# Kernel tuning notes

Hardware: AMD Instinct MI355X
Metric: run time of the kernel (lower is better)

Reference implementation:

```python
import jax, jax.numpy as jnp
import numpy as np

NUM_CODES = 128
CODE_DIM = 64
B, D, T = 64, 64, 8192


def setup_inputs() -> dict:
    key = jax.random.key(0)
    k1, k2 = jax.random.split(key)
    z_e = jax.random.normal(k1, (B, D, T), dtype=jnp.float32)
    centroids = jax.random.normal(k2, (NUM_CODES, CODE_DIM), dtype=jnp.float32)
    return {"z_e": z_e, "centroids": centroids}


def reference(z_e, centroids):
    b, d, t = z_e.shape
    K = centroids.shape[0]
    # [B, D, T] -> [B*T, D]
    z = jnp.transpose(z_e, (0, 2, 1)).reshape(b * t, d)
    # squared euclidean distances: ||z||^2 - 2 z C^T + ||C||^2  -> [N, K]
    dists = (
        jnp.sum(z * z, axis=1, keepdims=True)
        - 2.0 * (z @ centroids.T)
        + jnp.sum(centroids * centroids, axis=1)[None, :]
    )
    idx = jnp.argmin(dists, axis=1)  # [N]
    idx_bt = idx.reshape(b, t)[:, None, :]  # [B, 1, T]
    counts = jnp.bincount(idx, length=K).astype(jnp.float32)  # [K]
    p = jnp.maximum(counts / float(idx.size), 1e-12)
    H = -jnp.sum(p * jnp.log(p))
    perp = jnp.exp(H)
    usage = jnp.mean((counts > 0).astype(jnp.float32))
    return idx_bt, perp, usage
```

## Files before the change

### kernel.cpp

```cpp
#include <hip/hip_runtime.h>
#include <math.h>

#define NUM_CODES 128
#define CODE_DIM  64
#define B_ 64
#define D_ 64
#define T_ 8192
#define N_TOK (B_ * T_)

__global__ __launch_bounds__(128) void kmeans_prep(
    const float* __restrict__ centroids, float* __restrict__ c2h,
    unsigned int* __restrict__ counts)
{
    int k = threadIdx.x;
    if (k < NUM_CODES) {
        const float* cp = centroids + k * CODE_DIM;
        float s0 = 0.f, s1 = 0.f, s2 = 0.f, s3 = 0.f;
        #pragma unroll
        for (int d = 0; d < CODE_DIM; d += 4) {
            s0 = fmaf(cp[d + 0], cp[d + 0], s0);
            s1 = fmaf(cp[d + 1], cp[d + 1], s1);
            s2 = fmaf(cp[d + 2], cp[d + 2], s2);
            s3 = fmaf(cp[d + 3], cp[d + 3], s3);
        }
        c2h[k] = 0.5f * ((s0 + s1) + (s2 + s3));
        counts[k] = 0u;
    }
}

__global__ __launch_bounds__(256) void kmeans_assign(
    const float* __restrict__ z_e, const float* __restrict__ centroids,
    const float* __restrict__ c2h, unsigned int* __restrict__ counts,
    float* __restrict__ out_idx)
{
    const int n = blockIdx.x * 256 + threadIdx.x;
    const int b = n >> 13;
    const int t = n & (T_ - 1);

    const float* zp = z_e + (size_t)b * (size_t)(D_ * T_) + t;
    float z[64];
    #pragma unroll
    for (int d = 0; d < 64; ++d) z[d] = zp[(size_t)d * T_];

    float best = -3.4e38f;
    int   bi   = 0;

    for (int k = 0; k < NUM_CODES; ++k) {
        const float* cp = centroids + k * CODE_DIM;
        float a0 = -c2h[k], a1 = 0.f, a2 = 0.f, a3 = 0.f;
        #pragma unroll
        for (int d = 0; d < 64; d += 4) {
            a0 = fmaf(cp[d + 0], z[d + 0], a0);
            a1 = fmaf(cp[d + 1], z[d + 1], a1);
            a2 = fmaf(cp[d + 2], z[d + 2], a2);
            a3 = fmaf(cp[d + 3], z[d + 3], a3);
        }
        float m = (a0 + a1) + (a2 + a3);
        if (m > best) { best = m; bi = k; }
    }

    out_idx[n] = (float)bi;

    __shared__ unsigned int hist[NUM_CODES];
    if (threadIdx.x < NUM_CODES) hist[threadIdx.x] = 0u;
    __syncthreads();
    atomicAdd(&hist[bi], 1u);
    __syncthreads();
    if (threadIdx.x < NUM_CODES) {
        unsigned int h = hist[threadIdx.x];
        if (h) atomicAdd(&counts[threadIdx.x], h);
    }
}

__global__ __launch_bounds__(128) void kmeans_finalize(
    const unsigned int* __restrict__ counts, float* __restrict__ out)
{
    const int k = threadIdx.x;
    unsigned int c = counts[k];
    float p = fmaxf((float)c * (1.0f / (float)N_TOK), 1e-12f);
    float h = -p * logf(p);
    float u = (c > 0u) ? 1.0f : 0.0f;

    __shared__ float sh[NUM_CODES];
    __shared__ float su[NUM_CODES];
    sh[k] = h; su[k] = u;
    __syncthreads();
    for (int s = 64; s > 0; s >>= 1) {
        if (k < s) { sh[k] += sh[k + s]; su[k] += su[k + s]; }
        __syncthreads();
    }
    if (k == 0) {
        out[N_TOK + 0] = expf(sh[0]);
        out[N_TOK + 1] = su[0] * (1.0f / 128.f);
    }
}

extern "C" void kernel_launch(void* const* d_in, const int* in_sizes, int n_in,
                              void* d_out, int out_size, void* d_ws, size_t ws_size,
                              hipStream_t stream)
{
    const float* z_e       = (const float*)d_in[0];
    const float* centroids = (const float*)d_in[1];
    float* out = (float*)d_out;

    float*        c2h    = (float*)d_ws;
    unsigned int* counts = (unsigned int*)d_ws + NUM_CODES;

    kmeans_prep<<<1, 128, 0, stream>>>(centroids, c2h, counts);
    kmeans_assign<<<N_TOK / 256, 256, 0, stream>>>(z_e, centroids, c2h, counts, out);
    kmeans_finalize<<<1, 128, 0, stream>>>(counts, out);
}
```

Measured before the change: 310.7 us.

## Stage transposed centroids in LDS and split codes across waves per token

The prep kernel now also writes a transposed [D][K] copy of the centroids to the workspace. Each assign block loads that copy into shared memory, and each of its four waves handles 32 codes for the same 64 tokens, keeping per-code accumulators in registers. Partial argmins are then merged through shared memory. This replaces scalar centroid loads from global memory with vectorized LDS reads and removes the 64-float z register array, at the cost of four times as many blocks, a per-block 32KB LDS fill, and each z element being reloaded by all four waves.

```diff
diff --git a/kernel.cpp b/kernel.cpp
--- a/kernel.cpp
+++ b/kernel.cpp
@@ -10,65 +10,102 @@
 
 __global__ __launch_bounds__(128) void kmeans_prep(
     const float* __restrict__ centroids, float* __restrict__ c2h,
-    unsigned int* __restrict__ counts)
+    unsigned int* __restrict__ counts, float* __restrict__ ct)
 {
     int k = threadIdx.x;
-    if (k < NUM_CODES) {
-        const float* cp = centroids + k * CODE_DIM;
-        float s0 = 0.f, s1 = 0.f, s2 = 0.f, s3 = 0.f;
-        #pragma unroll
-        for (int d = 0; d < CODE_DIM; d += 4) {
-            s0 = fmaf(cp[d + 0], cp[d + 0], s0);
-            s1 = fmaf(cp[d + 1], cp[d + 1], s1);
-            s2 = fmaf(cp[d + 2], cp[d + 2], s2);
-            s3 = fmaf(cp[d + 3], cp[d + 3], s3);
-        }
-        c2h[k] = 0.5f * ((s0 + s1) + (s2 + s3));
-        counts[k] = 0u;
+    const float* cp = centroids + k * CODE_DIM;
+    float s0 = 0.f, s1 = 0.f, s2 = 0.f, s3 = 0.f;
+    #pragma unroll
+    for (int d = 0; d < CODE_DIM; d += 4) {
+        float c0 = cp[d], c1 = cp[d+1], c2 = cp[d+2], c3 = cp[d+3];
+        ct[(d+0)*NUM_CODES + k] = c0;
+        ct[(d+1)*NUM_CODES + k] = c1;
+        ct[(d+2)*NUM_CODES + k] = c2;
+        ct[(d+3)*NUM_CODES + k] = c3;
+        s0 = fmaf(c0, c0, s0); s1 = fmaf(c1, c1, s1);
+        s2 = fmaf(c2, c2, s2); s3 = fmaf(c3, c3, s3);
     }
+    c2h[k] = 0.5f * ((s0 + s1) + (s2 + s3));
+    counts[k] = 0u;
 }
 
-__global__ __launch_bounds__(256) void kmeans_assign(
-    const float* __restrict__ z_e, const float* __restrict__ centroids,
+__global__ __launch_bounds__(256, 4) void kmeans_assign(
+    const float* __restrict__ z_e, const float* __restrict__ ct,
     const float* __restrict__ c2h, unsigned int* __restrict__ counts,
     float* __restrict__ out_idx)
 {
-    const int n = blockIdx.x * 256 + threadIdx.x;
-    const int b = n >> 13;
-    const int t = n & (T_ - 1);
+    __shared__ float        ctl[CODE_DIM][NUM_CODES];
+    __shared__ float        c2l[NUM_CODES];
+    __shared__ float        sb[4][64];
+    __shared__ int          si[4][64];
+    __shared__ unsigned int hist[NUM_CODES];
 
+    const int tid   = threadIdx.x;
+    const int lane  = tid & 63;
+    const int w     = tid >> 6;
+    const int kbase = w * 32;
+
+    {
+        const float4* src = (const float4*)ct;
+        float4*       dst = (float4*)(&ctl[0][0]);
+        #pragma unroll
+        for (int r = 0; r < 8; ++r) dst[r * 256 + tid] = src[r * 256 + tid];
+        if (tid < NUM_CODES) { c2l[tid] = c2h[tid]; hist[tid] = 0u; }
+    }
+    __syncthreads();
+
+    const int n0 = blockIdx.x * 64;
+    const int b  = n0 >> 13;
+    const int t  = (n0 & (T_ - 1)) + lane;
     const float* zp = z_e + (size_t)b * (size_t)(D_ * T_) + t;
-    float z[64];
+
+    float acc0[32], acc1[32];
     #pragma unroll
-    for (int d = 0; d < 64; ++d) z[d] = zp[(size_t)d * T_];
+    for (int i = 0; i < 32; ++i) { acc0[i] = -c2l[kbase + i]; acc1[i] = 0.f; }
 
-    float best = -3.4e38f;
-    int   bi   = 0;
-
-    for (int k = 0; k < NUM_CODES; ++k) {
-        const float* cp = centroids + k * CODE_DIM;
-        float a0 = -c2h[k], a1 = 0.f, a2 = 0.f, a3 = 0.f;
+    #pragma unroll 2
+    for (int d = 0; d < CODE_DIM; d += 2) {
+        float z0 = zp[(size_t)(d + 0) * T_];
+        float z1 = zp[(size_t)(d + 1) * T_];
+        const float4* c0 = (const float4*)(&ctl[d + 0][kbase]);
+        const float4* c1 = (const float4*)(&ctl[d + 1][kbase]);
         #pragma unroll
-        for (int d = 0; d < 64; d += 4) {
-            a0 = fmaf(cp[d + 0], z[d + 0], a0);
-            a1 = fmaf(cp[d + 1], z[d + 1], a1);
-            a2 = fmaf(cp[d + 2], z[d + 2], a2);
-            a3 = fmaf(cp[d + 3], z[d + 3], a3);
+        for (int q = 0; q < 8; ++q) {
+            float4 ca = c0[q], cb = c1[q];
+            acc0[4*q+0] = fmaf(ca.x, z0, acc0[4*q+0]);
+            acc0[4*q+1] = fmaf(ca.y, z0, acc0[4*q+1]);
+            acc0[4*q+2] = fmaf(ca.z, z0, acc0[4*q+2]);
+            acc0[4*q+3] = fmaf(ca.w, z0, acc0[4*q+3]);
+            acc1[4*q+0] = fmaf(cb.x, z1, acc1[4*q+0]);
+            acc1[4*q+1] = fmaf(cb.y, z1, acc1[4*q+1]);
+            acc1[4*q+2] = fmaf(cb.z, z1, acc1[4*q+2]);
+            acc1[4*q+3] = fmaf(cb.w, z1, acc1[4*q+3]);
         }
-        float m = (a0 + a1) + (a2 + a3);
-        if (m > best) { best = m; bi = k; }
     }
 
-    out_idx[n] = (float)bi;
+    float bA = -3.4e38f; int iA = kbase;
+    #pragma unroll
+    for (int i = 0; i < 32; ++i) {
+        float m = acc0[i] + acc1[i];
+        if (m > bA) { bA = m; iA = kbase + i; }
+    }
+    sb[w][lane] = bA; si[w][lane] = iA;
+    __syncthreads();
 
-    __shared__ unsigned int hist[NUM_CODES];
-    if (threadIdx.x < NUM_CODES) hist[threadIdx.x] = 0u;
+    if (w == 0) {
+        float bb = sb[0][lane]; int bi = si[0][lane];
+        #pragma unroll
+        for (int ww = 1; ww < 4; ++ww) {
+            float v = sb[ww][lane];
+            if (v > bb) { bb = v; bi = si[ww][lane]; }
+        }
+        out_idx[n0 + lane] = (float)bi;
+        atomicAdd(&hist[bi], 1u);
+    }
     __syncthreads();
-    atomicAdd(&hist[bi], 1u);
-    __syncthreads();
-    if (threadIdx.x < NUM_CODES) {
-        unsigned int h = hist[threadIdx.x];
-        if (h) atomicAdd(&counts[threadIdx.x], h);
+    if (tid < NUM_CODES) {
+        unsigned int h = hist[tid];
+        if (h) atomicAdd(&counts[tid], h);
     }
 }
 
@@ -105,8 +142,9 @@
 
     float*        c2h    = (float*)d_ws;
     unsigned int* counts = (unsigned int*)d_ws + NUM_CODES;
+    float*        ct     = (float*)d_ws + 2 * NUM_CODES;
 
-    kmeans_prep<<<1, 128, 0, stream>>>(centroids, c2h, counts);
-    kmeans_assign<<<N_TOK / 256, 256, 0, stream>>>(z_e, centroids, c2h, counts, out);
+    kmeans_prep<<<1, 128, 0, stream>>>(centroids, c2h, counts, ct);
+    kmeans_assign<<<N_TOK / 64, 256, 0, stream>>>(z_e, ct, c2h, counts, out);
     kmeans_finalize<<<1, 128, 0, stream>>>(counts, out);
 }
```

Result: slower. 389.1 us (+25.2%).

## Stage centroids in LDS and use float4 broadcast reads in assign loop

Applied to the files above, without the earlier changes.

Each block copies the full 32KB centroid table and half-norms into shared memory, overlapping that copy with the per-thread z loads. The distance loop then reads centroids as float4 from LDS instead of scalar global/constant loads, with two accumulators and an unroll of 2. The occupancy hint is set to 4 blocks per CU. This cuts global/scalar load traffic in the inner loop, at the cost of 32KB LDS per block, which limits blocks per CU and changes the FP summation order slightly.

```diff
diff --git a/kernel.cpp b/kernel.cpp
--- a/kernel.cpp
+++ b/kernel.cpp
@@ -13,62 +13,74 @@
     unsigned int* __restrict__ counts)
 {
     int k = threadIdx.x;
-    if (k < NUM_CODES) {
-        const float* cp = centroids + k * CODE_DIM;
-        float s0 = 0.f, s1 = 0.f, s2 = 0.f, s3 = 0.f;
-        #pragma unroll
-        for (int d = 0; d < CODE_DIM; d += 4) {
-            s0 = fmaf(cp[d + 0], cp[d + 0], s0);
-            s1 = fmaf(cp[d + 1], cp[d + 1], s1);
-            s2 = fmaf(cp[d + 2], cp[d + 2], s2);
-            s3 = fmaf(cp[d + 3], cp[d + 3], s3);
-        }
-        c2h[k] = 0.5f * ((s0 + s1) + (s2 + s3));
-        counts[k] = 0u;
+    const float* cp = centroids + k * CODE_DIM;
+    float s0 = 0.f, s1 = 0.f, s2 = 0.f, s3 = 0.f;
+    #pragma unroll
+    for (int d = 0; d < CODE_DIM; d += 4) {
+        s0 = fmaf(cp[d + 0], cp[d + 0], s0);
+        s1 = fmaf(cp[d + 1], cp[d + 1], s1);
+        s2 = fmaf(cp[d + 2], cp[d + 2], s2);
+        s3 = fmaf(cp[d + 3], cp[d + 3], s3);
     }
+    c2h[k] = 0.5f * ((s0 + s1) + (s2 + s3));
+    counts[k] = 0u;
 }
 
-__global__ __launch_bounds__(256) void kmeans_assign(
+__global__ __launch_bounds__(256, 4) void kmeans_assign(
     const float* __restrict__ z_e, const float* __restrict__ centroids,
     const float* __restrict__ c2h, unsigned int* __restrict__ counts,
     float* __restrict__ out_idx)
 {
-    const int n = blockIdx.x * 256 + threadIdx.x;
+    __shared__ float        cl[NUM_CODES * CODE_DIM];
+    __shared__ float        c2l[NUM_CODES];
+    __shared__ unsigned int hist[NUM_CODES];
+
+    const int tid = threadIdx.x;
+
+    {
+        const float4* src = (const float4*)centroids;
+        float4*       dst = (float4*)cl;
+        #pragma unroll
+        for (int r = 0; r < 8; ++r) dst[r * 256 + tid] = src[r * 256 + tid];
+        if (tid < NUM_CODES) { c2l[tid] = c2h[tid]; hist[tid] = 0u; }
+    }
+
+    const int n = blockIdx.x * 256 + tid;
     const int b = n >> 13;
     const int t = n & (T_ - 1);
-
     const float* zp = z_e + (size_t)b * (size_t)(D_ * T_) + t;
     float z[64];
     #pragma unroll
     for (int d = 0; d < 64; ++d) z[d] = zp[(size_t)d * T_];
 
+    __syncthreads();
+
     float best = -3.4e38f;
     int   bi   = 0;
 
+    #pragma unroll 2
     for (int k = 0; k < NUM_CODES; ++k) {
-        const float* cp = centroids + k * CODE_DIM;
-        float a0 = -c2h[k], a1 = 0.f, a2 = 0.f, a3 = 0.f;
+        const float4* cp4 = (const float4*)(cl + k * CODE_DIM);
+        float a0 = -c2l[k], a1 = 0.f;
         #pragma unroll
-        for (int d = 0; d < 64; d += 4) {
-            a0 = fmaf(cp[d + 0], z[d + 0], a0);
-            a1 = fmaf(cp[d + 1], z[d + 1], a1);
-            a2 = fmaf(cp[d + 2], z[d + 2], a2);
-            a3 = fmaf(cp[d + 3], z[d + 3], a3);
+        for (int q = 0; q < 16; ++q) {
+            float4 c = cp4[q];
+            a0 = fmaf(c.x, z[4*q + 0], a0);
+            a1 = fmaf(c.y, z[4*q + 1], a1);
+            a0 = fmaf(c.z, z[4*q + 2], a0);
+            a1 = fmaf(c.w, z[4*q + 3], a1);
         }
-        float m = (a0 + a1) + (a2 + a3);
+        float m = a0 + a1;
         if (m > best) { best = m; bi = k; }
     }
 
     out_idx[n] = (float)bi;
 
-    __shared__ unsigned int hist[NUM_CODES];
-    if (threadIdx.x < NUM_CODES) hist[threadIdx.x] = 0u;
-    __syncthreads();
     atomicAdd(&hist[bi], 1u);
     __syncthreads();
-    if (threadIdx.x < NUM_CODES) {
-        unsigned int h = hist[threadIdx.x];
-        if (h) atomicAdd(&counts[threadIdx.x], h);
+    if (tid < NUM_CODES) {
+        unsigned int h = hist[tid];
+        if (h) atomicAdd(&counts[tid], h);
     }
 }
 
```

Result: faster. 302.4 us (-2.7%).
